# Optimization experiments

Hardware: AMD Instinct MI355X
Metric: run time of the kernel (lower is better)

Reference implementation:

```python
import jax, jax.numpy as jnp
import numpy as np

N = 50000      # nodes
E = 800000     # edges (before self-loops)
FEAT = 128     # input feature dim F
HID = 32       # per-head hidden H
HEADS = 8      # n_head
C = 40         # classes
NEG_SLOPE = 0.2


def setup_inputs() -> dict:
    key = jax.random.key(0)
    ks = jax.random.split(key, 12)
    x = jax.random.normal(ks[0], (N, FEAT), jnp.float32)
    edge_index = jax.random.randint(ks[1], (2, E), 0, N, jnp.int32)
    s1 = 1.0 / np.sqrt(FEAT)
    s2 = 1.0 / np.sqrt(HEADS * HID)
    W1 = jax.random.normal(ks[2], (FEAT, HEADS * HID), jnp.float32) * s1
    a1_src = jax.random.normal(ks[3], (HEADS, HID), jnp.float32) * s2
    a1_dst = jax.random.normal(ks[4], (HEADS, HID), jnp.float32) * s2
    b1 = jnp.zeros((HEADS * HID,), jnp.float32)
    W2 = jax.random.normal(ks[5], (HEADS * HID, HEADS * HID), jnp.float32) * s2
    a2_src = jax.random.normal(ks[6], (HEADS, HID), jnp.float32) * s2
    a2_dst = jax.random.normal(ks[7], (HEADS, HID), jnp.float32) * s2
    b2 = jnp.zeros((HEADS * HID,), jnp.float32)
    Wc = jax.random.normal(ks[8], (HEADS * HID, C), jnp.float32) * s2
    bc = jnp.zeros((C,), jnp.float32)
    return {"x": x, "edge_index": edge_index,
            "W1": W1, "a1_src": a1_src, "a1_dst": a1_dst, "b1": b1,
            "W2": W2, "a2_src": a2_src, "a2_dst": a2_dst, "b2": b2,
            "Wc": Wc, "bc": bc}


def gat_conv(x, src, dst, W, a_src, a_dst, b):
    # x: [N, F_in] -> per-head features [N, heads, H]
    n = x.shape[0]
    xh = (x @ W).reshape(n, HEADS, HID)
    alpha_s = jnp.einsum('nhd,hd->nh', xh, a_src)   # [N, heads]
    alpha_d = jnp.einsum('nhd,hd->nh', xh, a_dst)   # [N, heads]
    e = alpha_s[src] + alpha_d[dst]                  # [E, heads]
    e = jnp.where(e > 0, e, NEG_SLOPE * e)           # LeakyReLU(0.2)
    # softmax over incoming edges grouped by destination node
    emax = jax.ops.segment_max(e, dst, num_segments=n)
    ex = jnp.exp(e - emax[dst])
    denom = jax.ops.segment_sum(ex, dst, num_segments=n)
    alpha = ex / denom[dst]                          # [E, heads]
    msg = xh[src] * alpha[:, :, None]                # [E, heads, H]
    out = jax.ops.segment_sum(msg, dst, num_segments=n)
    return out.reshape(n, HEADS * HID) + b


def reference(x, edge_index, W1, a1_src, a1_dst, b1, W2, a2_src, a2_dst, b2, Wc, bc):
    # PyG GATConv adds self-loops by default
    loops = jnp.arange(N, dtype=edge_index.dtype)
    ei = jnp.concatenate([edge_index, jnp.stack([loops, loops])], axis=1)
    src, dst = ei[0], ei[1]
    h = gat_conv(x, src, dst, W1, a1_src, a1_dst, b1)
    h = jax.nn.relu(h)
    h = gat_conv(h, src, dst, W2, a2_src, a2_dst, b2)
    h = jax.nn.relu(h)
    return h @ Wc + bc
```

## Files before the change

### kernel.cpp

```cpp
#include <hip/hip_runtime.h>
#include <math.h>

#define NNODES 50000
#define NEDGES 800000
#define NTOT   850000
#define NHEAD  8
#define HDIM   32
#define HHD    256
#define NCLS   40
#define NEG_SLOPE 0.2f

typedef _Float16 half4 __attribute__((ext_vector_type(4)));
typedef _Float16 half8 __attribute__((ext_vector_type(8)));
typedef float f32x16 __attribute__((ext_vector_type(16)));
typedef unsigned short u16;


__global__ void k_init_counts(int* __restrict__ counts) {
    int i = blockIdx.x * 256 + threadIdx.x;
    if (i < NNODES) counts[i] = 1;
}

__global__ void k_count(const int* __restrict__ ei, int* __restrict__ counts) {
    int i = blockIdx.x * 256 + threadIdx.x;
    if (i < NEDGES) atomicAdd(&counts[ei[NEDGES + i]], 1);
}

__global__ __launch_bounds__(256) void k_scan1(const int* __restrict__ counts,
                                               int* __restrict__ partial,
                                               int* __restrict__ bsums) {
    __shared__ int lds[256];
    int t = threadIdx.x;
    int i = blockIdx.x * 256 + t;
    int v = (i < NNODES) ? counts[i] : 0;
    lds[t] = v;
    __syncthreads();
    for (int off = 1; off < 256; off <<= 1) {
        int add = (t >= off) ? lds[t - off] : 0;
        __syncthreads();
        lds[t] += add;
        __syncthreads();
    }
    if (i < NNODES) partial[i] = lds[t] - v;
    if (t == 255) bsums[blockIdx.x] = lds[255];
}

__global__ __launch_bounds__(256) void k_scan2(const int* __restrict__ bsums,
                                               int* __restrict__ boff, int nb) {
    __shared__ int lds[256];
    int t = threadIdx.x;
    int v = (t < nb) ? bsums[t] : 0;
    lds[t] = v;
    __syncthreads();
    for (int off = 1; off < 256; off <<= 1) {
        int add = (t >= off) ? lds[t - off] : 0;
        __syncthreads();
        lds[t] += add;
        __syncthreads();
    }
    if (t < nb) boff[t] = lds[t] - v;
}

__global__ void k_scan3(int* __restrict__ row_ptr, const int* __restrict__ boff,
                        int* __restrict__ cursor) {
    int i = blockIdx.x * 256 + threadIdx.x;
    if (i < NNODES) {
        int r = row_ptr[i] + boff[blockIdx.x];
        row_ptr[i] = r;
        cursor[i] = r;
    }
    if (i == 0) row_ptr[NNODES] = NTOT;
}

__global__ void k_scatter(const int* __restrict__ ei, int* __restrict__ cursor,
                          int* __restrict__ esrc) {
    int i = blockIdx.x * 256 + threadIdx.x;
    if (i < NEDGES) {
        int s = ei[i];
        int d = ei[NEDGES + i];
        int pos = atomicAdd(&cursor[d], 1);
        esrc[pos] = s;
    } else if (i < NTOT) {
        int n = i - NEDGES;
        int pos = atomicAdd(&cursor[n], 1);
        esrc[pos] = n;
    }
}

__global__ void k_prep_w(const float* __restrict__ W, _Float16* __restrict__ Wt,
                         int K, int Nc, int Npad) {
    int idx = blockIdx.x * 256 + threadIdx.x;
    if (idx >= Npad * K) return;
    int n = idx / K, k = idx - n * K;
    float w = (n < Nc) ? W[(size_t)k * Nc + n] : 0.f;
    Wt[idx] = (_Float16)w;
}

#define TBM 128
#define TBN 128
#define TBK 32
#define APAD 34

template <typename AT>
__global__ __launch_bounds__(256) void k_mfma_gemm(
    const AT* __restrict__ A,
    const _Float16* __restrict__ Wt,
    const float* __restrict__ bias,
    _Float16* __restrict__ Ch,
    float* __restrict__ Cf,
    int M, int K, int NcReal, int ldc)
{
    constexpr bool A_IS_F32 = sizeof(AT) == 4;
    __shared__ _Float16 Ah[TBM][APAD];
    int t = threadIdx.x;
    int lane = t & 63;
    int wid = t >> 6;
    int wr = wid >> 1, wc = wid & 1;
    int rowBase = blockIdx.y * TBM;
    int colBase = blockIdx.x * TBN;

    int arow = t >> 1;
    int akoff = (t & 1) * 16;
    bool arow_ok = (rowBase + arow) < M;
    const AT* aptr = A + (size_t)(rowBase + arow) * K + akoff;

    f32x16 acc[2][2];
    #pragma unroll
    for (int i = 0; i < 2; ++i)
        #pragma unroll
        for (int j = 0; j < 2; ++j)
            #pragma unroll
            for (int r = 0; r < 16; ++r) acc[i][j][r] = 0.f;

    float4 aregf[4];
    half8  aregh[2];
    auto load_a = [&](const AT* ap) {
        if constexpr (A_IS_F32) {
            #pragma unroll
            for (int i = 0; i < 4; ++i)
                aregf[i] = arow_ok ? *reinterpret_cast<const float4*>((const float*)ap + i * 4)
                                   : float4{0.f, 0.f, 0.f, 0.f};
        } else {
            #pragma unroll
            for (int i = 0; i < 2; ++i)
                aregh[i] = arow_ok ? *reinterpret_cast<const half8*>((const _Float16*)ap + i * 8)
                                   : half8{0, 0, 0, 0, 0, 0, 0, 0};
        }
    };
    load_a(aptr);

    for (int k0 = 0; k0 < K; k0 += TBK) {
        if constexpr (A_IS_F32) {
            half8 h0, h1;
            #pragma unroll
            for (int c = 0; c < 4; ++c) {
                float4 v = aregf[c];
                if (c < 2) {
                    h0[c * 4 + 0] = (_Float16)v.x; h0[c * 4 + 1] = (_Float16)v.y;
                    h0[c * 4 + 2] = (_Float16)v.z; h0[c * 4 + 3] = (_Float16)v.w;
                } else {
                    h1[(c - 2) * 4 + 0] = (_Float16)v.x; h1[(c - 2) * 4 + 1] = (_Float16)v.y;
                    h1[(c - 2) * 4 + 2] = (_Float16)v.z; h1[(c - 2) * 4 + 3] = (_Float16)v.w;
                }
            }
            *reinterpret_cast<half8*>(&Ah[arow][akoff])     = h0;
            *reinterpret_cast<half8*>(&Ah[arow][akoff + 8]) = h1;
        } else {
            *reinterpret_cast<half8*>(&Ah[arow][akoff])     = aregh[0];
            *reinterpret_cast<half8*>(&Ah[arow][akoff + 8]) = aregh[1];
        }
        __syncthreads();
        if (k0 + TBK < K) load_a(aptr + k0 + TBK);
        #pragma unroll
        for (int sub = 0; sub < 2; ++sub) {
            int kfo = sub * 16 + (lane >> 5) * 8;
            half8 ah[2];
            #pragma unroll
            for (int rt = 0; rt < 2; ++rt) {
                int r = wr * 64 + rt * 32 + (lane & 31);
                ah[rt] = *reinterpret_cast<const half8*>(&Ah[r][kfo]);
            }
            half8 bh[2];
            #pragma unroll
            for (int ct = 0; ct < 2; ++ct) {
                int n = colBase + wc * 64 + ct * 32 + (lane & 31);
                bh[ct] = *reinterpret_cast<const half8*>(Wt + (size_t)n * K + k0 + kfo);
            }
            #pragma unroll
            for (int rt = 0; rt < 2; ++rt)
                #pragma unroll
                for (int ct = 0; ct < 2; ++ct)
                    acc[rt][ct] = __builtin_amdgcn_mfma_f32_32x32x16_f16(
                        ah[rt], bh[ct], acc[rt][ct], 0, 0, 0);
        }
        __syncthreads();
    }

    #pragma unroll
    for (int rt = 0; rt < 2; ++rt)
        #pragma unroll
        for (int ct = 0; ct < 2; ++ct) {
            int col = colBase + wc * 64 + ct * 32 + (lane & 31);
            #pragma unroll
            for (int r = 0; r < 16; ++r) {
                int row = rowBase + wr * 64 + rt * 32 +
                          (r & 3) + 8 * (r >> 2) + 4 * (lane >> 5);
                if (row >= M) continue;
                float v = acc[rt][ct][r];
                if (Ch) {
                    Ch[(size_t)row * ldc + col] = (_Float16)v;
                } else if (col < NcReal) {
                    Cf[(size_t)row * ldc + col] = v + bias[col];
                }
            }
        }
}

__global__ void k_alpha(const _Float16* __restrict__ xh,
                        const float* __restrict__ a_src,
                        const float* __restrict__ a_dst,
                        float* __restrict__ alpha_s,
                        float* __restrict__ alpha_d) {
    int idx = blockIdx.x * 256 + threadIdx.x;
    if (idx >= NNODES * NHEAD) return;
    int node = idx >> 3, h = idx & 7;
    const half4* p  = reinterpret_cast<const half4*>(xh + (size_t)node * HHD + h * HDIM);
    const float4* ps = reinterpret_cast<const float4*>(a_src + h * HDIM);
    const float4* pd = reinterpret_cast<const float4*>(a_dst + h * HDIM);
    float ss = 0.f, sd = 0.f;
    #pragma unroll
    for (int q = 0; q < 8; ++q) {
        half4 hv = p[q];
        float4 s4 = ps[q], d4 = pd[q];
        float vx = (float)hv.x, vy = (float)hv.y, vz = (float)hv.z, vw = (float)hv.w;
        ss += vx * s4.x + vy * s4.y + vz * s4.z + vw * s4.w;
        sd += vx * d4.x + vy * d4.y + vz * d4.z + vw * d4.w;
    }
    alpha_s[idx] = ss;
    alpha_d[idx] = sd;
}

__global__ __launch_bounds__(256) void k_agg(const _Float16* __restrict__ xh,
                                             const float* __restrict__ alpha_s,
                                             const float* __restrict__ alpha_d,
                                             const int* __restrict__ row_ptr,
                                             const int* __restrict__ esrc,
                                             const float* __restrict__ bias,
                                             _Float16* __restrict__ out) {
    int wave = blockIdx.x * 4 + (threadIdx.x >> 6);
    int node = wave * 2 + ((threadIdx.x & 63) >> 5);
    if (node >= NNODES) return;
    int l = threadIdx.x & 31;
    int h = l >> 2;
    int beg = row_ptr[node], end = row_ptr[node + 1];
    float ad = alpha_d[node * NHEAD + h];
    float acc[8] = {};
    float ssum = 0.f;
    int i = beg;
    for (; i + 3 < end; i += 4) {
        int s0 = esrc[i], s1 = esrc[i + 1], s2 = esrc[i + 2], s3 = esrc[i + 3];
        float e0 = alpha_s[s0 * NHEAD + h] + ad;
        float e1 = alpha_s[s1 * NHEAD + h] + ad;
        float e2 = alpha_s[s2 * NHEAD + h] + ad;
        float e3 = alpha_s[s3 * NHEAD + h] + ad;
        half8 v0 = *reinterpret_cast<const half8*>(xh + (size_t)s0 * HHD + l * 8);
        half8 v1 = *reinterpret_cast<const half8*>(xh + (size_t)s1 * HHD + l * 8);
        half8 v2 = *reinterpret_cast<const half8*>(xh + (size_t)s2 * HHD + l * 8);
        half8 v3 = *reinterpret_cast<const half8*>(xh + (size_t)s3 * HHD + l * 8);
        e0 = (e0 > 0.f) ? e0 : NEG_SLOPE * e0;
        e1 = (e1 > 0.f) ? e1 : NEG_SLOPE * e1;
        e2 = (e2 > 0.f) ? e2 : NEG_SLOPE * e2;
        e3 = (e3 > 0.f) ? e3 : NEG_SLOPE * e3;
        float p0 = __expf(e0), p1 = __expf(e1), p2 = __expf(e2), p3 = __expf(e3);
        ssum += (p0 + p1) + (p2 + p3);
        #pragma unroll
        for (int d = 0; d < 8; ++d)
            acc[d] += p0 * (float)v0[d] + p1 * (float)v1[d] +
                      p2 * (float)v2[d] + p3 * (float)v3[d];
    }
    for (; i < end; ++i) {
        int s0 = esrc[i];
        float e0 = alpha_s[s0 * NHEAD + h] + ad;
        half8 v0 = *reinterpret_cast<const half8*>(xh + (size_t)s0 * HHD + l * 8);
        e0 = (e0 > 0.f) ? e0 : NEG_SLOPE * e0;
        float p0 = __expf(e0);
        ssum += p0;
        #pragma unroll
        for (int d = 0; d < 8; ++d)
            acc[d] += p0 * (float)v0[d];
    }
    float inv = 1.f / ssum;
    float4 b0 = *reinterpret_cast<const float4*>(bias + l * 8);
    float4 b1 = *reinterpret_cast<const float4*>(bias + l * 8 + 4);
    float bb[8] = {b0.x, b0.y, b0.z, b0.w, b1.x, b1.y, b1.z, b1.w};
    half8 r;
    #pragma unroll
    for (int d = 0; d < 8; ++d)
        r[d] = (_Float16)fmaxf(acc[d] * inv + bb[d], 0.f);
    *reinterpret_cast<half8*>(out + (size_t)node * HHD + l * 8) = r;
}


extern "C" void kernel_launch(void* const* d_in, const int* in_sizes, int n_in,
                              void* d_out, int out_size, void* d_ws, size_t ws_size,
                              hipStream_t stream) {
    const float* x   = (const float*)d_in[0];
    const int*   ei  = (const int*)  d_in[1];
    const float* W1  = (const float*)d_in[2];
    const float* a1s = (const float*)d_in[3];
    const float* a1d = (const float*)d_in[4];
    const float* b1  = (const float*)d_in[5];
    const float* W2  = (const float*)d_in[6];
    const float* a2s = (const float*)d_in[7];
    const float* a2d = (const float*)d_in[8];
    const float* b2  = (const float*)d_in[9];
    const float* Wc  = (const float*)d_in[10];
    const float* bc  = (const float*)d_in[11];
    float* out = (float*)d_out;

    char* ws = (char*)d_ws;
    size_t off = 0;
    auto alloc = [&](size_t bytes) -> void* {
        void* p = ws + off;
        off += (bytes + 255) & ~(size_t)255;
        return p;
    };
    _Float16* xh_h   = (_Float16*)alloc((size_t)NNODES * HHD * 2);
    _Float16* hbuf_h = (_Float16*)alloc((size_t)NNODES * HHD * 2);
    float* as_   = (float*)alloc((size_t)NNODES * NHEAD * 4);
    float* ad_   = (float*)alloc((size_t)NNODES * NHEAD * 4);
    int* counts  = (int*)alloc((size_t)NNODES * 4);
    int* row_ptr = (int*)alloc((size_t)(NNODES + 1) * 4);
    int* cursor  = (int*)alloc((size_t)NNODES * 4);
    int* esrc    = (int*)alloc((size_t)NTOT * 4);
    int* bsums   = (int*)alloc(256 * 4);
    int* boff    = (int*)alloc(256 * 4);
    _Float16* w1t = (_Float16*)alloc((size_t)HHD * 128 * 2);
    _Float16* w2t = (_Float16*)alloc((size_t)HHD * HHD * 2);
    _Float16* wct = (_Float16*)alloc((size_t)TBN * HHD * 2);
    (void)ws_size; (void)in_sizes; (void)n_in; (void)out_size;

    int gn = (NNODES + 255) / 256;
    int ge = (NEDGES + 255) / 256;
    int gt = (NTOT + 255) / 256;

    k_init_counts<<<gn, 256, 0, stream>>>(counts);
    k_count<<<ge, 256, 0, stream>>>(ei, counts);
    k_scan1<<<gn, 256, 0, stream>>>(counts, row_ptr, bsums);
    k_scan2<<<1, 256, 0, stream>>>(bsums, boff, gn);
    k_scan3<<<gn, 256, 0, stream>>>(row_ptr, boff, cursor);
    k_scatter<<<gt, 256, 0, stream>>>(ei, cursor, esrc);

    k_prep_w<<<(HHD * 128 + 255) / 256, 256, 0, stream>>>(W1, w1t, 128, HHD, HHD);
    k_prep_w<<<(HHD * HHD + 255) / 256, 256, 0, stream>>>(W2, w2t, HHD, HHD, HHD);
    k_prep_w<<<(TBN * HHD + 255) / 256, 256, 0, stream>>>(Wc, wct, HHD, NCLS, TBN);

    dim3 gHid(HHD / TBN, (NNODES + TBM - 1) / TBM);
    dim3 gCls(1, (NNODES + TBM - 1) / TBM);
    int ga = (NNODES * NHEAD + 255) / 256;
    int gagg = NNODES / 8;

    k_mfma_gemm<float><<<gHid, 256, 0, stream>>>(x, w1t, nullptr, xh_h, nullptr,
                                                 NNODES, 128, HHD, HHD);
    k_alpha<<<ga, 256, 0, stream>>>(xh_h, a1s, a1d, as_, ad_);
    k_agg<<<gagg, 256, 0, stream>>>(xh_h, as_, ad_, row_ptr, esrc, b1, hbuf_h);

    k_mfma_gemm<_Float16><<<gHid, 256, 0, stream>>>(hbuf_h, w2t, nullptr, xh_h, nullptr,
                                                    NNODES, HHD, HHD, HHD);
    k_alpha<<<ga, 256, 0, stream>>>(xh_h, a2s, a2d, as_, ad_);
    k_agg<<<gagg, 256, 0, stream>>>(xh_h, as_, ad_, row_ptr, esrc, b2, hbuf_h);

    k_mfma_gemm<_Float16><<<gCls, 256, 0, stream>>>(hbuf_h, wct, bc, nullptr, out,
                                                    NNODES, HHD, NCLS, NCLS);
}
```

Measured before the change: 351.2 us.

## Fuse attention logits into GEMM epilogue and pre-swizzle weights into MFMA fragments

Removes the separate k_alpha kernels. The GEMM now writes each output tile to LDS and computes the per-head source and destination attention dot products in its epilogue. Weights are repacked once, by a single prep kernel, into a fragment-major fp16 layout so each lane's B operand load is contiguous. This removes two launches and a full re-read of xh. The cost is extra LDS, an added barrier, and a serial per-thread dot-product loop in the epilogue.

```diff
diff --git a/kernel.cpp b/kernel.cpp
--- a/kernel.cpp
+++ b/kernel.cpp
@@ -87,13 +87,26 @@
     }
 }
 
-__global__ void k_prep_w(const float* __restrict__ W, _Float16* __restrict__ Wt,
-                         int K, int Nc, int Npad) {
-    int idx = blockIdx.x * 256 + threadIdx.x;
-    if (idx >= Npad * K) return;
-    int n = idx / K, k = idx - n * K;
-    float w = (n < Nc) ? W[(size_t)k * Nc + n] : 0.f;
-    Wt[idx] = (_Float16)w;
+__global__ void k_prep_all(const float* __restrict__ W1, const float* __restrict__ W2,
+                           const float* __restrict__ Wc,
+                           _Float16* __restrict__ w1t, _Float16* __restrict__ w2t,
+                           _Float16* __restrict__ wct) {
+    int gid = blockIdx.x * 256 + threadIdx.x;
+    if (gid >= 256 * 64) return;
+    int frag = gid >> 6, l = gid & 63;
+    const float* W; _Float16* Wt; int K, Nc, fkn, fbase;
+    if (frag < 64)       { W = W1; Wt = w1t; K = 128; Nc = 256; fkn = 8;  fbase = 0; }
+    else if (frag < 192) { W = W2; Wt = w2t; K = 256; Nc = 256; fkn = 16; fbase = 64; }
+    else                 { W = Wc; Wt = wct; K = 256; Nc = 40;  fkn = 16; fbase = 192; }
+    int f = frag - fbase;
+    int fn = f / fkn, fk = f - fn * fkn;
+    int n = fn * 32 + (l & 31);
+    int k = fk * 16 + ((l >> 5) << 3);
+    half8 v;
+    #pragma unroll
+    for (int j = 0; j < 8; ++j)
+        v[j] = (n < Nc) ? (_Float16)W[(size_t)(k + j) * Nc + n] : (_Float16)0.f;
+    *reinterpret_cast<half8*>(Wt + ((size_t)f * 64 + l) * 8) = v;
 }
 
 #define TBM 128
@@ -101,17 +114,23 @@
 #define TBK 32
 #define APAD 34
 
-template <typename AT>
+template <typename AT, bool FUSE_ALPHA>
 __global__ __launch_bounds__(256) void k_mfma_gemm(
     const AT* __restrict__ A,
     const _Float16* __restrict__ Wt,
     const float* __restrict__ bias,
     _Float16* __restrict__ Ch,
     float* __restrict__ Cf,
+    const float* __restrict__ a_src,
+    const float* __restrict__ a_dst,
+    float* __restrict__ alpha_s,
+    float* __restrict__ alpha_d,
     int M, int K, int NcReal, int ldc)
 {
     constexpr bool A_IS_F32 = sizeof(AT) == 4;
+    constexpr int CT_ROWS = FUSE_ALPHA ? TBM : 1;
     __shared__ _Float16 Ah[TBM][APAD];
+    __shared__ _Float16 Ct[CT_ROWS][TBN + 4];
     int t = threadIdx.x;
     int lane = t & 63;
     int wid = t >> 6;
@@ -123,6 +142,14 @@
     int akoff = (t & 1) * 16;
     bool arow_ok = (rowBase + arow) < M;
     const AT* aptr = A + (size_t)(rowBase + arow) * K + akoff;
+
+    int fkn = K >> 4;
+    size_t bbase[2];
+    #pragma unroll
+    for (int ct = 0; ct < 2; ++ct) {
+        int fn = blockIdx.x * 4 + wc * 2 + ct;
+        bbase[ct] = ((size_t)fn * fkn) * 512 + (size_t)lane * 8;
+    }
 
     f32x16 acc[2][2];
     #pragma unroll
@@ -181,11 +208,10 @@
                 ah[rt] = *reinterpret_cast<const half8*>(&Ah[r][kfo]);
             }
             half8 bh[2];
-            #pragma unroll
-            for (int ct = 0; ct < 2; ++ct) {
-                int n = colBase + wc * 64 + ct * 32 + (lane & 31);
-                bh[ct] = *reinterpret_cast<const half8*>(Wt + (size_t)n * K + k0 + kfo);
-            }
+            int fidx = (k0 >> 4) + sub;
+            #pragma unroll
+            for (int ct = 0; ct < 2; ++ct)
+                bh[ct] = *reinterpret_cast<const half8*>(Wt + bbase[ct] + (size_t)fidx * 512);
             #pragma unroll
             for (int rt = 0; rt < 2; ++rt)
                 #pragma unroll
@@ -200,44 +226,46 @@
     for (int rt = 0; rt < 2; ++rt)
         #pragma unroll
         for (int ct = 0; ct < 2; ++ct) {
-            int col = colBase + wc * 64 + ct * 32 + (lane & 31);
+            int lcol = wc * 64 + ct * 32 + (lane & 31);
+            int col = colBase + lcol;
             #pragma unroll
             for (int r = 0; r < 16; ++r) {
-                int row = rowBase + wr * 64 + rt * 32 +
-                          (r & 3) + 8 * (r >> 2) + 4 * (lane >> 5);
+                int lrow = wr * 64 + rt * 32 + (r & 3) + 8 * (r >> 2) + 4 * (lane >> 5);
+                int row = rowBase + lrow;
+                float v = acc[rt][ct][r];
+                _Float16 hv = (_Float16)v;
+                if constexpr (FUSE_ALPHA) Ct[lrow][lcol] = hv;
                 if (row >= M) continue;
-                float v = acc[rt][ct][r];
                 if (Ch) {
-                    Ch[(size_t)row * ldc + col] = (_Float16)v;
+                    Ch[(size_t)row * ldc + col] = hv;
                 } else if (col < NcReal) {
                     Cf[(size_t)row * ldc + col] = v + bias[col];
                 }
             }
         }
-}
-
-__global__ void k_alpha(const _Float16* __restrict__ xh,
-                        const float* __restrict__ a_src,
-                        const float* __restrict__ a_dst,
-                        float* __restrict__ alpha_s,
-                        float* __restrict__ alpha_d) {
-    int idx = blockIdx.x * 256 + threadIdx.x;
-    if (idx >= NNODES * NHEAD) return;
-    int node = idx >> 3, h = idx & 7;
-    const half4* p  = reinterpret_cast<const half4*>(xh + (size_t)node * HHD + h * HDIM);
-    const float4* ps = reinterpret_cast<const float4*>(a_src + h * HDIM);
-    const float4* pd = reinterpret_cast<const float4*>(a_dst + h * HDIM);
-    float ss = 0.f, sd = 0.f;
-    #pragma unroll
-    for (int q = 0; q < 8; ++q) {
-        half4 hv = p[q];
-        float4 s4 = ps[q], d4 = pd[q];
-        float vx = (float)hv.x, vy = (float)hv.y, vz = (float)hv.z, vw = (float)hv.w;
-        ss += vx * s4.x + vy * s4.y + vz * s4.z + vw * s4.w;
-        sd += vx * d4.x + vy * d4.y + vz * d4.z + vw * d4.w;
-    }
-    alpha_s[idx] = ss;
-    alpha_d[idx] = sd;
+
+    if constexpr (FUSE_ALPHA) {
+        __syncthreads();
+        #pragma unroll
+        for (int idx = t; idx < TBM * 4; idx += 256) {
+            int lrow = idx >> 2, hoff = idx & 3;
+            int grow = rowBase + lrow;
+            if (grow < M) {
+                int h = blockIdx.x * 4 + hoff;
+                const float* as4 = a_src + h * HDIM;
+                const float* ad4 = a_dst + h * HDIM;
+                float ss = 0.f, sd = 0.f;
+                #pragma unroll
+                for (int j = 0; j < HDIM; ++j) {
+                    float v = (float)Ct[lrow][hoff * 32 + j];
+                    ss += v * as4[j];
+                    sd += v * ad4[j];
+                }
+                alpha_s[grow * NHEAD + h] = ss;
+                alpha_d[grow * NHEAD + h] = sd;
+            }
+        }
+    }
 }
 
 __global__ __launch_bounds__(256) void k_agg(const _Float16* __restrict__ xh,
@@ -335,9 +363,9 @@
     int* esrc    = (int*)alloc((size_t)NTOT * 4);
     int* bsums   = (int*)alloc(256 * 4);
     int* boff    = (int*)alloc(256 * 4);
-    _Float16* w1t = (_Float16*)alloc((size_t)HHD * 128 * 2);
-    _Float16* w2t = (_Float16*)alloc((size_t)HHD * HHD * 2);
-    _Float16* wct = (_Float16*)alloc((size_t)TBN * HHD * 2);
+    _Float16* w1t = (_Float16*)alloc((size_t)64 * 64 * 8 * 2);
+    _Float16* w2t = (_Float16*)alloc((size_t)128 * 64 * 8 * 2);
+    _Float16* wct = (_Float16*)alloc((size_t)64 * 64 * 8 * 2);
     (void)ws_size; (void)in_sizes; (void)n_in; (void)out_size;
 
     int gn = (NNODES + 255) / 256;
@@ -351,25 +379,21 @@
     k_scan3<<<gn, 256, 0, stream>>>(row_ptr, boff, cursor);
     k_scatter<<<gt, 256, 0, stream>>>(ei, cursor, esrc);
 
-    k_prep_w<<<(HHD * 128 + 255) / 256, 256, 0, stream>>>(W1, w1t, 128, HHD, HHD);
-    k_prep_w<<<(HHD * HHD + 255) / 256, 256, 0, stream>>>(W2, w2t, HHD, HHD, HHD);
-    k_prep_w<<<(TBN * HHD + 255) / 256, 256, 0, stream>>>(Wc, wct, HHD, NCLS, TBN);
+    k_prep_all<<<64, 256, 0, stream>>>(W1, W2, Wc, w1t, w2t, wct);
 
     dim3 gHid(HHD / TBN, (NNODES + TBM - 1) / TBM);
     dim3 gCls(1, (NNODES + TBM - 1) / TBM);
-    int ga = (NNODES * NHEAD + 255) / 256;
     int gagg = NNODES / 8;
 
-    k_mfma_gemm<float><<<gHid, 256, 0, stream>>>(x, w1t, nullptr, xh_h, nullptr,
-                                                 NNODES, 128, HHD, HHD);
-    k_alpha<<<ga, 256, 0, stream>>>(xh_h, a1s, a1d, as_, ad_);
+    k_mfma_gemm<float, true><<<gHid, 256, 0, stream>>>(
+        x, w1t, nullptr, xh_h, nullptr, a1s, a1d, as_, ad_, NNODES, 128, HHD, HHD);
     k_agg<<<gagg, 256, 0, stream>>>(xh_h, as_, ad_, row_ptr, esrc, b1, hbuf_h);
 
-    k_mfma_gemm<_Float16><<<gHid, 256, 0, stream>>>(hbuf_h, w2t, nullptr, xh_h, nullptr,
-                                                    NNODES, HHD, HHD, HHD);
-    k_alpha<<<ga, 256, 0, stream>>>(xh_h, a2s, a2d, as_, ad_);
+    k_mfma_gemm<_Float16, true><<<gHid, 256, 0, stream>>>(
+        hbuf_h, w2t, nullptr, xh_h, nullptr, a2s, a2d, as_, ad_, NNODES, HHD, HHD, HHD);
     k_agg<<<gagg, 256, 0, stream>>>(xh_h, as_, ad_, row_ptr, esrc, b2, hbuf_h);
 
-    k_mfma_gemm<_Float16><<<gCls, 256, 0, stream>>>(hbuf_h, wct, bc, nullptr, out,
-                                                    NNODES, HHD, NCLS, NCLS);
-}
+    k_mfma_gemm<_Float16, false><<<gCls, 256, 0, stream>>>(
+        hbuf_h, wct, bc, nullptr, out, nullptr, nullptr, nullptr, nullptr,
+        NNODES, HHD, NCLS, NCLS);
+}
```

After: 336.4 us. 1.04x faster.
